# Optimization experiments

Measured on AMD Instinct MI355X. Metric: run time of the kernel, lower is better.

The kernel has to match this reference:

```python
import jax, jax.numpy as jnp
import numpy as np

B, H, T, D = 2, 8, 2048, 64
STATE = H * D  # 512

def setup_inputs() -> dict:
    key = jax.random.key(0)
    kq, kk, kv, kw, kl = jax.random.split(key, 5)
    q = jax.random.normal(kq, (B * H, T, D), jnp.float32)
    k = jax.random.normal(kk, (B * H, T, D), jnp.float32)
    v = jax.random.normal(kv, (B * H, T, D), jnp.float32)
    # causal position mask: True = masked (future positions)
    position_mask = jnp.triu(jnp.ones((T, T), dtype=bool), 1)
    # per-batch source lengths in [T//2, T]; True = padding (masked)
    lengths = jax.random.randint(kl, (B,), T // 2, T + 1)
    src_length_mask = jnp.arange(T)[None, :] >= lengths[:, None]
    W_merge = jax.random.normal(kw, (STATE, STATE), jnp.float32) / np.sqrt(STATE)
    return {"q": q, "k": k, "v": v, "position_mask": position_mask,
            "src_length_mask": src_length_mask, "W_merge": W_merge}

def reference(q, k, v, position_mask, src_length_mask, W_merge):
    bb, n_dest, d = q.shape              # bb = B*H
    n_batch = src_length_mask.shape[0]
    n_heads = bb // n_batch
    scale = 1.0 / np.sqrt(d)
    # [bb, T_dest, T_src] full score matrix (as in the torch bmm)
    logits = jnp.einsum('btd,bsd->bts', q, k) * scale
    logits = logits.reshape(n_batch, n_heads, n_dest, -1)
    logits = jnp.where(position_mask[None, None], -jnp.inf, logits)
    logits = jnp.where(src_length_mask[:, None, None, :], -jnp.inf, logits)
    scores = jax.nn.softmax(logits, axis=-1).reshape(bb, n_dest, -1)
    # dropout p=0 (eval) -> identity
    out = jnp.einsum('bts,bsd->btd', scores, v)
    out = out.reshape(n_batch, n_heads, n_dest, d).transpose(0, 2, 1, 3)
    out = out.reshape(n_batch, n_dest, n_heads * d)
    return out @ W_merge.T  # bias-free Linear merge
```

## Files before the change

### kernel.cpp

```cpp
#include <hip/hip_runtime.h>

#define TT 2048
#define DD 64
#define NSTATE 512

typedef __attribute__((ext_vector_type(8))) short short8;
typedef __attribute__((ext_vector_type(4))) short short4v;
typedef __attribute__((ext_vector_type(4))) float f4;

__device__ __forceinline__ short f2bf(float x) {
  union { float f; unsigned u; } c; c.f = x;
  unsigned r = (c.u + 0x7FFFu + ((c.u >> 16) & 1u)) >> 16;
  return (short)r;
}

__device__ __forceinline__ bool mask_at(const void* p, bool u8, int idx) {
  return u8 ? (((const unsigned char*)p)[idx] != 0)
            : (((const int*)p)[idx] != 0);
}

__device__ __forceinline__ void gld16(const void* g, void* l) {
  __builtin_amdgcn_global_load_lds(
      (const __attribute__((address_space(1))) void*)g,
      (__attribute__((address_space(3))) void*)l, 16, 0, 0);
}

__global__ __launch_bounds__(256)
void prep_kernel(const float* __restrict__ k, const float* __restrict__ v,
                 const float* __restrict__ W, const void* __restrict__ posmask,
                 const void* __restrict__ srcmask,
                 unsigned short* __restrict__ Wb, unsigned short* __restrict__ Kimg,
                 unsigned short* __restrict__ VTimg, int* __restrict__ lenbuf) {
  const int bidx = blockIdx.x;
  const int tid = threadIdx.x;
  if (bidx < 512) {
    const int bh = bidx >> 5, tile = bidx & 31;
    const float* kp = k + (bh * TT + tile * 64) * DD;
    unsigned short* dst = Kimg + (bh * 32 + tile) * 4096;
#pragma unroll
    for (int t2 = 0; t2 < 2; ++t2) {
      int j = tid + t2 * 256;
      int c8 = j >> 6, r6 = j & 63;
      int kb = c8 >> 1, cc = c8 & 1, qd = r6 >> 4, klo = r6 & 15;
      int key = kb * 16 + klo, dg = cc * 4 + qd;
      f4 a0 = *(const f4*)(kp + key * DD + dg * 8);
      f4 a1 = *(const f4*)(kp + key * DD + dg * 8 + 4);
      short8 o;
      o[0]=f2bf(a0[0]); o[1]=f2bf(a0[1]); o[2]=f2bf(a0[2]); o[3]=f2bf(a0[3]);
      o[4]=f2bf(a1[0]); o[5]=f2bf(a1[1]); o[6]=f2bf(a1[2]); o[7]=f2bf(a1[3]);
      *(short8*)(dst + j * 8) = o;
    }
    __shared__ float Vt[64][65];
    const float* vp = v + (bh * TT + tile * 64) * DD;
    {
      int key = tid >> 2, c0 = (tid & 3) * 16;
#pragma unroll
      for (int i = 0; i < 4; ++i) {
        f4 x = *(const f4*)(vp + key * DD + c0 + i * 4);
        Vt[key][c0 + i * 4 + 0] = x[0];
        Vt[key][c0 + i * 4 + 1] = x[1];
        Vt[key][c0 + i * 4 + 2] = x[2];
        Vt[key][c0 + i * 4 + 3] = x[3];
      }
    }
    __syncthreads();
    unsigned short* vd = VTimg + (bh * 32 + tile) * 5120;
#pragma unroll
    for (int t2 = 0; t2 < 3; ++t2) {
      int j = tid + t2 * 256;
      if (j < 640) {
        int d = j / 10, sc = j - d * 10;
        short8 o = (short8){0,0,0,0,0,0,0,0};
        if (sc < 8) {
#pragma unroll
          for (int i = 0; i < 8; ++i) o[i] = f2bf(Vt[sc * 8 + i][d]);
        }
        *(short8*)(vd + d * 80 + sc * 8) = o;
      }
    }
  } else if (bidx < 768) {
    int i = ((bidx - 512) * 256 + tid) * 4;
    f4 x = *(const f4*)(W + i);
    short4v o;
    o[0]=f2bf(x[0]); o[1]=f2bf(x[1]); o[2]=f2bf(x[2]); o[3]=f2bf(x[3]);
    *(short4v*)(Wb + i) = o;
  } else {
    const int wv = tid >> 6, lane = tid & 63;
    if (wv < 2) {
      const bool u8 = (((const unsigned char*)posmask)[1] != 0);
      int pos = 1024 + lane * 16;
      bool m1 = mask_at(srcmask, u8, wv * TT + pos);
      unsigned long long bal = __ballot(m1);
      int cur = bal ? (1024 + (__ffsll((unsigned long long)bal) - 1) * 16) : 2048;
      int prev = cur - 16;
      bool m2 = false;
      if (lane < 16) {
        int pos2 = prev + 1 + lane;
        m2 = (pos2 < TT) ? mask_at(srcmask, u8, wv * TT + pos2) : true;
      }
      unsigned long long bal2 = __ballot(m2);
      int len = prev + 1 + (__ffsll((unsigned long long)bal2) - 1);
      if (lane == 0) lenbuf[wv] = len;
    }
  }
}

__global__ __launch_bounds__(128)
void attn_kernel(const float* __restrict__ q, const unsigned short* __restrict__ Kimg,
                 const unsigned short* __restrict__ VTimg,
                 const int* __restrict__ lenbuf, unsigned short* __restrict__ merged) {
  const int bid = blockIdx.x;
  const int bh = bid & 15;
  const int qraw = bid >> 4;
  const int qt = (qraw & 1) ? (63 - (qraw >> 1)) : (qraw >> 1);
  const int b = bh >> 3, h = bh & 7;
  const int tid = threadIdx.x;
  const int w = tid >> 6, lane = tid & 63;
  const int lane_lo = lane & 15, quad = lane >> 4;
  const int q0 = qt * 32 + w * 16;
  const int len = lenbuf[b];
  const int n_st = min((qt >> 1) + 1, (len + 63) >> 6);

  __shared__ __attribute__((aligned(16))) unsigned short Klds[2][4096];
  __shared__ __attribute__((aligned(16))) unsigned short Vlds[2][5120];

  short8 qf[2];
  {
    const float* qrow = q + ((bh * TT) + q0 + lane_lo) * DD;
#pragma unroll
    for (int c = 0; c < 2; ++c) {
      int d0 = c * 32 + quad * 8;
      f4 a0 = *(const f4*)(qrow + d0);
      f4 a1 = *(const f4*)(qrow + d0 + 4);
      short8 t;
      t[0]=f2bf(a0[0]*0.125f); t[1]=f2bf(a0[1]*0.125f);
      t[2]=f2bf(a0[2]*0.125f); t[3]=f2bf(a0[3]*0.125f);
      t[4]=f2bf(a1[0]*0.125f); t[5]=f2bf(a1[1]*0.125f);
      t[6]=f2bf(a1[2]*0.125f); t[7]=f2bf(a1[3]*0.125f);
      qf[c] = t;
    }
  }

  float l_lane = 0.f;
  f4 O[4];
#pragma unroll
  for (int d = 0; d < 4; ++d) O[d] = (f4){0.f, 0.f, 0.f, 0.f};

  const char* kbase = (const char*)(Kimg + (size_t)bh * 32 * 4096);
  const char* vbase = (const char*)(VTimg + (size_t)bh * 32 * 5120);

  auto stage = [&](int st, int bufi) {
    const char* ks = kbase + st * 8192 + w * 4096 + lane * 16;
    char* kl = (char*)&Klds[bufi][0] + w * 4096 + lane * 16;
#pragma unroll
    for (int i = 0; i < 4; ++i) gld16(ks + i * 1024, kl + i * 1024);
    const char* vs = vbase + st * 10240 + w * 5120 + lane * 16;
    char* vl = (char*)&Vlds[bufi][0] + w * 5120 + lane * 16;
#pragma unroll
    for (int i = 0; i < 5; ++i) gld16(vs + i * 1024, vl + i * 1024);
  };

  stage(0, 0);
  __syncthreads();

  for (int st = 0; st < n_st; ++st) {
    const int bufc = st & 1;
    if (st + 1 < n_st) stage(st + 1, bufc ^ 1);
    const unsigned short* Kl = Klds[bufc];
    const unsigned short* Vl = Vlds[bufc];
    const int s0 = st * 64;

    f4 ST[4];
#pragma unroll
    for (int sb = 0; sb < 4; ++sb) {
      f4 acc = (f4){0.f, 0.f, 0.f, 0.f};
#pragma unroll
      for (int c = 0; c < 2; ++c) {
        short8 kf = *(const short8*)&Kl[((sb * 2 + c) * 64 + lane) * 8];
        acc = __builtin_amdgcn_mfma_f32_16x16x32_bf16(kf, qf[c], acc, 0, 0, 0);
      }
      ST[sb] = acc;
    }

    const bool edge = (st == (qt >> 1)) || (s0 + 64 > len);
    const int tq = q0 + lane_lo;
    short4v pf[4];
#pragma unroll
    for (int sb = 0; sb < 4; ++sb) {
#pragma unroll
      for (int r = 0; r < 4; ++r) {
        float p = __expf(ST[sb][r]);
        if (edge) {
          int s = s0 + sb * 16 + quad * 4 + r;
          if (s > tq || s >= len) p = 0.f;
        }
        l_lane += p;
        pf[sb][r] = f2bf(p);
      }
    }

#pragma unroll
    for (int db = 0; db < 4; ++db) {
      f4 acc = O[db];
#pragma unroll
      for (int sb = 0; sb < 4; ++sb) {
        short4v vf = *(const short4v*)&Vl[(db * 16 + lane_lo) * 80 + sb * 16 + quad * 4];
        acc = __builtin_amdgcn_mfma_f32_16x16x16bf16_1k(pf[sb], vf, acc, 0, 0, 0);
      }
      O[db] = acc;
    }
    __syncthreads();
  }

  l_lane += __shfl_xor(l_lane, 16);
  l_lane += __shfl_xor(l_lane, 32);
  float inv = 1.0f / l_lane;
  float invr[4];
#pragma unroll
  for (int r = 0; r < 4; ++r) invr[r] = __shfl(inv, quad * 4 + r);
#pragma unroll
  for (int db = 0; db < 4; ++db)
#pragma unroll
    for (int r = 0; r < 4; ++r) {
      int t = q0 + quad * 4 + r;
      merged[((b * TT) + t) * NSTATE + h * DD + db * 16 + lane_lo] =
          (unsigned short)f2bf(O[db][r] * invr[r]);
    }
}

__global__ __launch_bounds__(256)
void merge_kernel(const unsigned short* __restrict__ A,
                  const unsigned short* __restrict__ Wb,
                  float* __restrict__ out) {
  __shared__ __attribute__((aligned(16))) unsigned short Wl[64 * 512];
  const int tid = threadIdx.x;
  const int n0 = blockIdx.x * 64, m0 = blockIdx.y * 64;
  {
    int row = tid >> 2, cb = (tid & 3) * 16;
    const unsigned short* src = Wb + (n0 + row) * NSTATE;
#pragma unroll
    for (int j = 0; j < 16; ++j) {
      int c = cb + j;
      int phys = c ^ (row & 7);
      *(short8*)&Wl[row * 512 + phys * 8] = *(const short8*)(src + c * 8);
    }
  }
  __syncthreads();

  const int w = tid >> 6, lane = tid & 63;
  const int lo16 = lane & 15, quad = lane >> 4;
  const int m = m0 + w * 16;
  f4 acc[4];
#pragma unroll
  for (int nf = 0; nf < 4; ++nf) acc[nf] = (f4){0.f, 0.f, 0.f, 0.f};
  const unsigned short* arow = A + (m + lo16) * NSTATE + quad * 8;
#pragma unroll 4
  for (int k0 = 0; k0 < NSTATE; k0 += 32) {
    short8 af = *(const short8*)(arow + k0);
#pragma unroll
    for (int nf = 0; nf < 4; ++nf) {
      int n = nf * 16 + lo16;
      int phys = ((k0 >> 3) + quad) ^ (n & 7);
      short8 bf = *(const short8*)&Wl[n * 512 + phys * 8];
      acc[nf] = __builtin_amdgcn_mfma_f32_16x16x32_bf16(af, bf, acc[nf], 0, 0, 0);
    }
  }
#pragma unroll
  for (int nf = 0; nf < 4; ++nf)
#pragma unroll
    for (int r = 0; r < 4; ++r)
      out[(m + quad * 4 + r) * NSTATE + n0 + nf * 16 + lo16] = acc[nf][r];
}

extern "C" void kernel_launch(void* const* d_in, const int* in_sizes, int n_in,
                              void* d_out, int out_size, void* d_ws, size_t ws_size,
                              hipStream_t stream) {
  (void)in_sizes; (void)n_in; (void)out_size; (void)ws_size;
  const float* q = (const float*)d_in[0];
  const float* k = (const float*)d_in[1];
  const float* v = (const float*)d_in[2];
  const void* posm = d_in[3];
  const void* srcm = d_in[4];
  const float* W = (const float*)d_in[5];
  float* out = (float*)d_out;

  unsigned short* merged = (unsigned short*)d_ws;
  unsigned short* Wb     = merged + 2097152;
  unsigned short* Kimg   = Wb + 262144;
  unsigned short* VTimg  = Kimg + 2097152;
  int* lenbuf = (int*)(VTimg + 2621440);

  prep_kernel<<<dim3(769), dim3(256), 0, stream>>>(k, v, W, posm, srcm,
                                                   Wb, Kimg, VTimg, lenbuf);
  attn_kernel<<<dim3(1024), dim3(128), 0, stream>>>(q, Kimg, VTimg, lenbuf, merged);
  merge_kernel<<<dim3(8, 64), dim3(256), 0, stream>>>(merged, Wb, out);
}
```

Baseline: 136.8 us.

## Split attention over key chunks and add a combine kernel

```diff
diff --git a/kernel.cpp b/kernel.cpp
--- a/kernel.cpp
+++ b/kernel.cpp
@@ -64,19 +64,18 @@
       }
     }
     __syncthreads();
-    unsigned short* vd = VTimg + (bh * 32 + tile) * 5120;
-#pragma unroll
-    for (int t2 = 0; t2 < 3; ++t2) {
-      int j = tid + t2 * 256;
-      if (j < 640) {
-        int d = j / 10, sc = j - d * 10;
-        short8 o = (short8){0,0,0,0,0,0,0,0};
-        if (sc < 8) {
-#pragma unroll
-          for (int i = 0; i < 8; ++i) o[i] = f2bf(Vt[sc * 8 + i][d]);
-        }
-        *(short8*)(vd + d * 80 + sc * 8) = o;
-      }
+    unsigned short* vd = VTimg + (bh * 32 + tile) * 4096;
+#pragma unroll
+    for (int t2 = 0; t2 < 2; ++t2) {
+      int cc = tid + t2 * 256;
+      int tI = cc >> 5, w5 = cc & 31;
+      int dl = w5 >> 1, sg = w5 & 1;
+      int db = tI >> 2, sb = tI & 3;
+      int d = db * 16 + dl;
+      short8 o;
+#pragma unroll
+      for (int i = 0; i < 8; ++i) o[i] = f2bf(Vt[sb * 16 + sg * 8 + i][d]);
+      *(short8*)(vd + tI * 256 + dl * 16 + sg * 8) = o;
     }
   } else if (bidx < 768) {
     int i = ((bidx - 512) * 256 + tid) * 4;
@@ -108,21 +107,27 @@
 __global__ __launch_bounds__(128)
 void attn_kernel(const float* __restrict__ q, const unsigned short* __restrict__ Kimg,
                  const unsigned short* __restrict__ VTimg,
-                 const int* __restrict__ lenbuf, unsigned short* __restrict__ merged) {
+                 const int* __restrict__ lenbuf,
+                 float* __restrict__ Opart, float* __restrict__ lpart) {
   const int bid = blockIdx.x;
-  const int bh = bid & 15;
-  const int qraw = bid >> 4;
-  const int qt = (qraw & 1) ? (63 - (qraw >> 1)) : (qraw >> 1);
-  const int b = bh >> 3, h = bh & 7;
+  const int chunk = bid >> 10;
+  const int rem = bid & 1023;
+  const int bh = rem & 15;
+  const int qt = rem >> 4;
+  const int b = bh >> 3, h = bh & 7; (void)h;
+  const int len = lenbuf[b];
+  const int n_st = min((qt >> 1) + 1, (len + 63) >> 6);
+  const int c0 = chunk * 8;
+  if (c0 >= n_st) return;
+  const int cend = min(n_st, c0 + 8);
+
   const int tid = threadIdx.x;
   const int w = tid >> 6, lane = tid & 63;
   const int lane_lo = lane & 15, quad = lane >> 4;
   const int q0 = qt * 32 + w * 16;
-  const int len = lenbuf[b];
-  const int n_st = min((qt >> 1) + 1, (len + 63) >> 6);
 
   __shared__ __attribute__((aligned(16))) unsigned short Klds[2][4096];
-  __shared__ __attribute__((aligned(16))) unsigned short Vlds[2][5120];
+  __shared__ __attribute__((aligned(16))) unsigned short Vlds[2][4096];
 
   short8 qf[2];
   {
@@ -147,25 +152,25 @@
   for (int d = 0; d < 4; ++d) O[d] = (f4){0.f, 0.f, 0.f, 0.f};
 
   const char* kbase = (const char*)(Kimg + (size_t)bh * 32 * 4096);
-  const char* vbase = (const char*)(VTimg + (size_t)bh * 32 * 5120);
+  const char* vbase = (const char*)(VTimg + (size_t)bh * 32 * 4096);
 
   auto stage = [&](int st, int bufi) {
     const char* ks = kbase + st * 8192 + w * 4096 + lane * 16;
     char* kl = (char*)&Klds[bufi][0] + w * 4096 + lane * 16;
 #pragma unroll
     for (int i = 0; i < 4; ++i) gld16(ks + i * 1024, kl + i * 1024);
-    const char* vs = vbase + st * 10240 + w * 5120 + lane * 16;
-    char* vl = (char*)&Vlds[bufi][0] + w * 5120 + lane * 16;
-#pragma unroll
-    for (int i = 0; i < 5; ++i) gld16(vs + i * 1024, vl + i * 1024);
+    const char* vs = vbase + st * 8192 + w * 4096 + lane * 16;
+    char* vl = (char*)&Vlds[bufi][0] + w * 4096 + lane * 16;
+#pragma unroll
+    for (int i = 0; i < 4; ++i) gld16(vs + i * 1024, vl + i * 1024);
   };
 
-  stage(0, 0);
+  stage(c0, 0);
   __syncthreads();
 
-  for (int st = 0; st < n_st; ++st) {
-    const int bufc = st & 1;
-    if (st + 1 < n_st) stage(st + 1, bufc ^ 1);
+  for (int st = c0; st < cend; ++st) {
+    const int bufc = (st - c0) & 1;
+    if (st + 1 < cend) stage(st + 1, bufc ^ 1);
     const unsigned short* Kl = Klds[bufc];
     const unsigned short* Vl = Vlds[bufc];
     const int s0 = st * 64;
@@ -204,7 +209,7 @@
       f4 acc = O[db];
 #pragma unroll
       for (int sb = 0; sb < 4; ++sb) {
-        short4v vf = *(const short4v*)&Vl[(db * 16 + lane_lo) * 80 + sb * 16 + quad * 4];
+        short4v vf = *(const short4v*)&Vl[(db * 4 + sb) * 256 + lane_lo * 16 + quad * 4];
         acc = __builtin_amdgcn_mfma_f32_16x16x16bf16_1k(pf[sb], vf, acc, 0, 0, 0);
       }
       O[db] = acc;
@@ -214,18 +219,42 @@
 
   l_lane += __shfl_xor(l_lane, 16);
   l_lane += __shfl_xor(l_lane, 32);
-  float inv = 1.0f / l_lane;
-  float invr[4];
-#pragma unroll
-  for (int r = 0; r < 4; ++r) invr[r] = __shfl(inv, quad * 4 + r);
+
+  const int pid = (bh << 6) | qt;
+  float* ob = Opart + ((size_t)(pid * 4 + chunk)) * 2048;
 #pragma unroll
   for (int db = 0; db < 4; ++db)
 #pragma unroll
-    for (int r = 0; r < 4; ++r) {
-      int t = q0 + quad * 4 + r;
-      merged[((b * TT) + t) * NSTATE + h * DD + db * 16 + lane_lo] =
-          (unsigned short)f2bf(O[db][r] * invr[r]);
-    }
+    for (int r = 0; r < 4; ++r)
+      ob[(w * 16 + quad * 4 + r) * 64 + db * 16 + lane_lo] = O[db][r];
+  if (quad == 0)
+    lpart[(pid * 4 + chunk) * 32 + w * 16 + lane_lo] = l_lane;
+}
+
+__global__ __launch_bounds__(256)
+void combine_kernel(const float* __restrict__ Opart, const float* __restrict__ lpart,
+                    const int* __restrict__ lenbuf, unsigned short* __restrict__ merged) {
+  const int pid = blockIdx.x;
+  const int bh = pid >> 6, qt = pid & 63;
+  const int b = bh >> 3, h = bh & 7;
+  const int len = lenbuf[b];
+  const int n_st = min((qt >> 1) + 1, (len + 63) >> 6);
+  const int nch = min(4, (n_st + 7) >> 3);
+  const int tid = threadIdx.x;
+  const int qi = tid >> 3, dg = tid & 7;
+  const float* basep = Opart + (size_t)pid * 4 * 2048 + qi * 64 + dg * 8;
+  f4 a0 = (f4){0.f,0.f,0.f,0.f}, a1 = (f4){0.f,0.f,0.f,0.f};
+  float l = 0.f;
+  for (int ch = 0; ch < nch; ++ch) {
+    a0 += *(const f4*)(basep + ch * 2048);
+    a1 += *(const f4*)(basep + ch * 2048 + 4);
+    l += lpart[(pid * 4 + ch) * 32 + qi];
+  }
+  float inv = 1.0f / l;
+  short8 o;
+  o[0]=f2bf(a0[0]*inv); o[1]=f2bf(a0[1]*inv); o[2]=f2bf(a0[2]*inv); o[3]=f2bf(a0[3]*inv);
+  o[4]=f2bf(a1[0]*inv); o[5]=f2bf(a1[1]*inv); o[6]=f2bf(a1[2]*inv); o[7]=f2bf(a1[3]*inv);
+  *(short8*)&merged[((size_t)(b * TT) + qt * 32 + qi) * NSTATE + h * 64 + dg * 8] = o;
 }
 
 __global__ __launch_bounds__(256)
@@ -288,10 +317,14 @@
   unsigned short* Wb     = merged + 2097152;
   unsigned short* Kimg   = Wb + 262144;
   unsigned short* VTimg  = Kimg + 2097152;
-  int* lenbuf = (int*)(VTimg + 2621440);
+  float* Opart = (float*)(VTimg + 2097152);
+  float* lpart = Opart + (size_t)4096 * 2048;
+  int* lenbuf  = (int*)(lpart + 4096 * 32);
 
   prep_kernel<<<dim3(769), dim3(256), 0, stream>>>(k, v, W, posm, srcm,
                                                    Wb, Kimg, VTimg, lenbuf);
-  attn_kernel<<<dim3(1024), dim3(128), 0, stream>>>(q, Kimg, VTimg, lenbuf, merged);
+  attn_kernel<<<dim3(4096), dim3(128), 0, stream>>>(q, Kimg, VTimg, lenbuf,
+                                                    Opart, lpart);
+  combine_kernel<<<dim3(1024), dim3(256), 0, stream>>>(Opart, lpart, lenbuf, merged);
   merge_kernel<<<dim3(8, 64), dim3(256), 0, stream>>>(merged, Wb, out);
 }
```

Result: no change. 138.7 us (+1.4%).
